# Optimization experiments

Measured on AMD Instinct MI355X. Metric: run time of the kernel, lower is better.

The kernel has to match this reference:

```python
import jax, jax.numpy as jnp
import numpy as np
from jax import lax

B, L, D_MODEL = 4, 512, 256
N_LAYERS = 6
EXPAND = 2
D_INNER = EXPAND * D_MODEL  # 512
D_STATE = 16
D_CONV = 4
DT_RANK = (D_MODEL + 15) // 16  # 16
EPS = 1e-5


def silu(x):
    return x * jax.nn.sigmoid(x)


def rmsnorm(x, w):
    var = jnp.mean(x * x, axis=-1, keepdims=True)
    return x * lax.rsqrt(var + EPS) * w


def setup_inputs() -> dict:
    key = jax.random.key(0)
    ks = jax.random.split(key, 12)
    s = lambda *sh: 0.02
    inp = {
        "x": jax.random.normal(ks[0], (B, L, D_MODEL), dtype=jnp.float32),
        "norm_w": jnp.ones((N_LAYERS, D_MODEL), jnp.float32),
        "W_in": jax.random.normal(ks[1], (N_LAYERS, 2 * D_INNER, D_MODEL), jnp.float32) * 0.02,
        "b_in": jnp.zeros((N_LAYERS, 2 * D_INNER), jnp.float32),
        "conv_w": jax.random.normal(ks[2], (N_LAYERS, D_INNER, D_CONV), jnp.float32) * 0.2,
        "W_x": jax.random.normal(ks[3], (N_LAYERS, DT_RANK + 2 * D_STATE, D_INNER), jnp.float32) * 0.02,
        "dt_w": jax.random.normal(ks[4], (N_LAYERS, D_INNER, DT_RANK), jnp.float32) * 0.1,
        "dt_b": jax.random.uniform(ks[5], (N_LAYERS, D_INNER), jnp.float32, -4.0, -2.0),
        "A_log": jnp.log(jnp.broadcast_to(jnp.arange(1, D_STATE + 1, dtype=jnp.float32), (N_LAYERS, D_INNER, D_STATE))),
        "D": jnp.ones((N_LAYERS, D_INNER), jnp.float32),
        "W_out": jax.random.normal(ks[6], (N_LAYERS, D_MODEL, D_INNER), jnp.float32) * 0.02,
        "b_out": jnp.zeros((N_LAYERS, D_MODEL), jnp.float32),
    }
    return inp


def mamba_block(x, W_in, b_in, conv_w, W_x, dt_w, dt_b, A_log, D, W_out, b_out):
    # input projection -> (B, L, 2*d_inner)
    xz = jnp.einsum("bld,ed->ble", x, W_in) + b_in
    xin, z = xz[..., :D_INNER], xz[..., D_INNER:]
    # depthwise causal conv over time (groups = d_inner, left pad d_conv-1)
    xc = lax.conv_general_dilated(
        xin.transpose(0, 2, 1),            # (B, C, L)
        conv_w[:, None, :],                # (C, 1, K)
        window_strides=(1,),
        padding=[(D_CONV - 1, 0)],
        feature_group_count=D_INNER,
        dimension_numbers=("NCH", "OIH", "NCH"),
    ).transpose(0, 2, 1)
    u = silu(xc)                           # (B, L, d_inner)
    # data-dependent dt, B, C
    xdbc = jnp.einsum("bld,rd->blr", u, W_x)
    dt = xdbc[..., :DT_RANK]
    Bm = xdbc[..., DT_RANK:DT_RANK + D_STATE]
    Cm = xdbc[..., DT_RANK + D_STATE:]
    delta = jax.nn.softplus(jnp.einsum("blr,dr->bld", dt, dt_w) + dt_b)
    A = -jnp.exp(A_log)                    # (d_inner, d_state)
    dA = jnp.exp(jnp.einsum("bld,dn->bldn", delta, A))
    dBu = jnp.einsum("bld,bln->bldn", delta * u, Bm)
    # selective scan over time
    def step(h, inp):
        dA_t, dBu_t, C_t = inp
        h = dA_t * h + dBu_t               # (B, d_inner, d_state)
        y_t = jnp.einsum("bdn,bn->bd", h, C_t)
        return h, y_t
    h0 = jnp.zeros((B, D_INNER, D_STATE), x.dtype)
    _, ys = lax.scan(step, h0, (dA.transpose(1, 0, 2, 3), dBu.transpose(1, 0, 2, 3), Cm.transpose(1, 0, 2)))
    y = ys.transpose(1, 0, 2) + u * D      # skip connection D*u
    y = y * silu(z)
    return jnp.einsum("bld,md->blm", y, W_out) + b_out


def reference(x, norm_w, W_in, b_in, conv_w, W_x, dt_w, dt_b, A_log, D, W_out, b_out):
    for i in range(N_LAYERS):
        x = x + mamba_block(rmsnorm(x, norm_w[i]), W_in[i], b_in[i], conv_w[i], W_x[i], dt_w[i], dt_b[i], A_log[i], D[i], W_out[i], b_out[i])
    return x
```

## Files before the change

### kernel.cpp

```cpp
#include <hip/hip_runtime.h>
#include <hip/hip_bf16.h>

#define B_SZ 4
#define L_SZ 512
#define D_MODEL 256
#define D_INNER 512
#define D_STATE 16
#define DT_RANK 16
#define N_LAYERS 6
#define BL (B_SZ * L_SZ)

typedef __bf16 bf16_t;
typedef __bf16 bf16x8 __attribute__((ext_vector_type(8)));
typedef __bf16 bf16x4 __attribute__((ext_vector_type(4)));
typedef float  f32x4  __attribute__((ext_vector_type(4)));

__device__ __forceinline__ float row_allreduce16(float x)
{
    int v;
    v = __builtin_amdgcn_mov_dpp(__float_as_int(x), 0x121, 0xf, 0xf, true);
    x += __int_as_float(v);
    v = __builtin_amdgcn_mov_dpp(__float_as_int(x), 0x122, 0xf, 0xf, true);
    x += __int_as_float(v);
    v = __builtin_amdgcn_mov_dpp(__float_as_int(x), 0x124, 0xf, 0xf, true);
    x += __int_as_float(v);
    v = __builtin_amdgcn_mov_dpp(__float_as_int(x), 0x128, 0xf, 0xf, true);
    x += __int_as_float(v);
    return x;
}

__global__ __launch_bounds__(256) void cast3_kernel(
    const float* __restrict__ s0, const float* __restrict__ s1,
    const float* __restrict__ s2, bf16_t* __restrict__ dst,
    int n0, int n1, int n2)
{
    int i = blockIdx.x * 256 + threadIdx.x;
    const float* s; int off;
    if (i < n0)            { s = s0; off = i; }
    else if (i < n0 + n1)  { s = s1; off = i - n0; }
    else if (i < n0+n1+n2) { s = s2; off = i - n0 - n1; }
    else return;
    const float4 v = *(const float4*)(s + (size_t)off * 4);
    bf16x4 o;
    o[0] = (bf16_t)v.x; o[1] = (bf16_t)v.y;
    o[2] = (bf16_t)v.z; o[3] = (bf16_t)v.w;
    *(bf16x4*)(dst + (size_t)i * 4) = o;
}

__global__ __launch_bounds__(256) void rmsnorm_kernel(
    const float* __restrict__ x, const float* __restrict__ w,
    bf16_t* __restrict__ o)
{
    int row  = blockIdx.x * 4 + (threadIdx.x >> 6);
    int lane = threadIdx.x & 63;
    const float4 v = *(const float4*)(x + (size_t)row * D_MODEL + lane * 4);
    float ss = v.x * v.x + v.y * v.y + v.z * v.z + v.w * v.w;
    #pragma unroll
    for (int off = 32; off; off >>= 1) ss += __shfl_xor(ss, off);
    float rs = rsqrtf(ss * (1.f / D_MODEL) + 1e-5f);
    const float4 wv = *(const float4*)(w + lane * 4);
    bf16x4 ov;
    ov[0] = (bf16_t)(v.x * rs * wv.x);
    ov[1] = (bf16_t)(v.y * rs * wv.y);
    ov[2] = (bf16_t)(v.z * rs * wv.z);
    ov[3] = (bf16_t)(v.w * rs * wv.w);
    *(bf16x4*)(o + (size_t)row * D_MODEL + lane * 4) = ov;
}

template<int WM, int WN, int TM_T, int TN_T, int HAS_BIAS, int HAS_RES, int ZSPLIT>
__global__ __launch_bounds__(64 * WM * WN) void gemm_mfma_nt(
    const bf16_t* __restrict__ A, int lda,
    const bf16_t* __restrict__ Bw, int ldb,
    const float* __restrict__ bias,
    const float* __restrict__ R, int ldr,
    float* __restrict__ C, int ldc,
    float* __restrict__ Z,
    int K)
{
    constexpr int BK = 64;
    constexpr int BM = WM * TM_T * 16;
    constexpr int BN = WN * TN_T * 16;
    constexpr int NT = 64 * WM * WN;
    constexpr int LDK = BK + 8;
    __shared__ bf16_t As[BM][LDK];
    __shared__ bf16_t Bs[BN][LDK];

    const int tid  = threadIdx.x;
    const int wave = tid >> 6, lane = tid & 63;
    const int wm = wave / WN, wn = wave % WN;
    const int lm = lane & 15, quad = lane >> 4;
    const int m0 = blockIdx.y * BM, n0 = blockIdx.x * BN;

    f32x4 acc[TM_T][TN_T] = {};

    for (int k0 = 0; k0 < K; k0 += BK) {
        #pragma unroll
        for (int i = tid; i < BM * (BK / 8); i += NT) {
            int r = i >> 3, c8 = i & 7;
            *(bf16x8*)&As[r][c8 * 8] =
                *(const bf16x8*)(A + (size_t)(m0 + r) * lda + k0 + c8 * 8);
        }
        #pragma unroll
        for (int i = tid; i < BN * (BK / 8); i += NT) {
            int r = i >> 3, c8 = i & 7;
            *(bf16x8*)&Bs[r][c8 * 8] =
                *(const bf16x8*)(Bw + (size_t)(n0 + r) * ldb + k0 + c8 * 8);
        }
        __syncthreads();
        #pragma unroll
        for (int ks = 0; ks < BK / 32; ++ks) {
            bf16x8 af[TM_T], bfr[TN_T];
            #pragma unroll
            for (int i = 0; i < TM_T; ++i)
                af[i] = *(const bf16x8*)&As[wm * TM_T * 16 + i * 16 + lm][ks * 32 + quad * 8];
            #pragma unroll
            for (int j = 0; j < TN_T; ++j)
                bfr[j] = *(const bf16x8*)&Bs[wn * TN_T * 16 + j * 16 + lm][ks * 32 + quad * 8];
            #pragma unroll
            for (int i = 0; i < TM_T; ++i)
                #pragma unroll
                for (int j = 0; j < TN_T; ++j)
                    acc[i][j] = __builtin_amdgcn_mfma_f32_16x16x32_bf16(
                        af[i], bfr[j], acc[i][j], 0, 0, 0);
        }
        __syncthreads();
    }

    if (ZSPLIT && n0 >= D_INNER) {
        #pragma unroll
        for (int i = 0; i < TM_T; ++i) {
            int rowbase = m0 + wm * TM_T * 16 + i * 16 + quad * 4;
            #pragma unroll
            for (int j = 0; j < TN_T; ++j) {
                int col = n0 + wn * TN_T * 16 + j * 16 + lm;
                float4 o;
                #pragma unroll
                for (int r = 0; r < 4; ++r) {
                    float v = acc[i][j][r];
                    if (HAS_BIAS) v += bias[col];
                    ((float*)&o)[r] = v / (1.f + __expf(-v));
                }
                *(float4*)(Z + (size_t)(col - D_INNER) * BL + rowbase) = o;
            }
        }
        return;
    }

    #pragma unroll
    for (int i = 0; i < TM_T; ++i) {
        #pragma unroll
        for (int j = 0; j < TN_T; ++j) {
            int col = n0 + wn * TN_T * 16 + j * 16 + lm;
            #pragma unroll
            for (int r = 0; r < 4; ++r) {
                int rowm = m0 + wm * TM_T * 16 + i * 16 + quad * 4 + r;
                float v = acc[i][j][r];
                if (HAS_BIAS) v += bias[col];
                if (HAS_RES)  v += R[(size_t)rowm * ldr + col];
                C[(size_t)rowm * ldc + col] = v;
            }
        }
    }
}

__global__ __launch_bounds__(256) void wx_conv_kernel(
    const float* __restrict__ xzx,
    const float* __restrict__ cw,
    const bf16_t* __restrict__ Bw,
    float* __restrict__ uT,
    float* __restrict__ xdbcT)
{
    constexpr int K = 512;
    __shared__ float  xs[19][516];
    __shared__ bf16_t us[16][520];
    __shared__ f32x4  part[4][3][64];

    const int tid  = threadIdx.x;
    const int wave = tid >> 6, lane = tid & 63;
    const int lm = lane & 15, quad = lane >> 4;
    const int m0 = blockIdx.x * 16;

    for (int q = tid; q < 19 * 128; q += 256) {
        int rx = q >> 7, c4 = (q & 127) * 4;
        int mr = m0 - 3 + rx;
        float4 v = make_float4(0.f, 0.f, 0.f, 0.f);
        if (mr >= 0) v = *(const float4*)(xzx + (size_t)mr * K + c4);
        *(float4*)&xs[rx][c4] = v;
    }
    __syncthreads();

    #pragma unroll
    for (int it = 0; it < 8; ++it) {
        int item = tid + it * 256;
        int d = item >> 2, rg = item & 3;
        const float4 wv = *(const float4*)(cw + d * 4);
        float4 o;
        #pragma unroll
        for (int e = 0; e < 4; ++e) {
            int ro = rg * 4 + e;
            int t  = (m0 + ro) & (L_SZ - 1);
            float a = wv.w * xs[ro + 3][d];
            if (t >= 1) a += wv.z * xs[ro + 2][d];
            if (t >= 2) a += wv.y * xs[ro + 1][d];
            if (t >= 3) a += wv.x * xs[ro + 0][d];
            a = a / (1.f + __expf(-a));
            ((float*)&o)[e] = a;
            us[ro][d] = (bf16_t)a;
        }
        *(float4*)(uT + (size_t)d * BL + m0 + rg * 4) = o;
    }
    __syncthreads();

    f32x4 acc[3] = {};
    const int kb = wave * 128 + quad * 8;
    #pragma unroll
    for (int ks = 0; ks < 4; ++ks) {
        int k0 = kb + ks * 32;
        bf16x8 af = *(const bf16x8*)&us[lm][k0];
        #pragma unroll
        for (int j = 0; j < 3; ++j) {
            bf16x8 bfr = *(const bf16x8*)(Bw + (size_t)(j * 16 + lm) * K + k0);
            acc[j] = __builtin_amdgcn_mfma_f32_16x16x32_bf16(af, bfr, acc[j], 0, 0, 0);
        }
    }
    #pragma unroll
    for (int j = 0; j < 3; ++j) part[wave][j][lane] = acc[j];
    __syncthreads();

    if (tid < 192) {
        int j = tid >> 6, l = tid & 63;
        f32x4 s = part[0][j][l];
        s += part[1][j][l];
        s += part[2][j][l];
        s += part[3][j][l];
        int col = j * 16 + (l & 15);
        float4 v = make_float4(s[0], s[1], s[2], s[3]);
        *(float4*)(xdbcT + (size_t)col * BL + m0 + (l >> 4) * 4) = v;
    }
}

__global__ __launch_bounds__(1024, 4) void scan_kernel(
    const float* __restrict__ xdbcT,
    const float* __restrict__ uT,
    const float* __restrict__ szT,
    const float* __restrict__ dt_w,
    const float* __restrict__ dt_b,
    const float* __restrict__ A_log,
    const float* __restrict__ Dv,
    bf16_t* __restrict__ y)
{
    constexpr int TC = 32;
    constexpr int NW = L_SZ / TC;

    int blk  = blockIdx.x;
    int b    = blk >> 7;
    int dg   = blk & 127;
    int wave = threadIdx.x >> 6;
    int lane = threadIdx.x & 63;
    int d    = dg * 4 + (lane >> 4);
    int n    = lane & 15;

    __shared__ float lds_Ap[NW][64];
    __shared__ float lds_he[NW][64];

    float Adn = -__expf(A_log[d * D_STATE + n]);
    float Dd  = Dv[d];
    int r0 = b * L_SZ + wave * TC;

    const float* Brow = xdbcT  + (size_t)(DT_RANK + n) * BL;
    const float* Crow = xdbcT  + (size_t)(DT_RANK + D_STATE + n) * BL;
    const float* urow = uT     + (size_t)d * BL;
    const float* zrow = szT    + (size_t)d * BL;

    float myd[2];
    {
        float w16[16];
        #pragma unroll
        for (int k4 = 0; k4 < 4; ++k4) {
            float4 wv = *(const float4*)(dt_w + (size_t)d * 16 + k4 * 4);
            w16[k4*4+0] = wv.x; w16[k4*4+1] = wv.y;
            w16[k4*4+2] = wv.z; w16[k4*4+3] = wv.w;
        }
        float bdt = dt_b[d];
        #pragma unroll
        for (int g = 0; g < 2; ++g) {
            int t = r0 + g * 16 + n;
            float a = bdt;
            #pragma unroll
            for (int k = 0; k < 16; ++k)
                a += xdbcT[(size_t)k * BL + t] * w16[k];
            myd[g] = (a > 20.f) ? a : __logf(1.f + __expf(a));
        }
    }
    const int sbase = lane & 48;

    float hl[TC], Pl[TC];
    float h = 0.f, P = 1.f;
    #pragma unroll
    for (int g = 0; g < 2; ++g) {
        #pragma unroll
        for (int j4 = 0; j4 < 4; ++j4) {
            int rb = r0 + g * 16 + j4 * 4;
            f32x4 Bv = *(const f32x4*)(Brow + rb);
            f32x4 uv = *(const f32x4*)(urow + rb);
            float dA[4], dBu[4];
            #pragma unroll
            for (int k = 0; k < 4; ++k) {
                float dlj = __shfl(myd[g], sbase | (j4 * 4 + k));
                dA[k]  = __expf(dlj * Adn);
                dBu[k] = dlj * uv[k] * Bv[k];
            }
            #pragma unroll
            for (int k = 0; k < 4; ++k) {
                int t = g * 16 + j4 * 4 + k;
                h = dA[k] * h + dBu[k];
                P *= dA[k];
                hl[t] = h;
                Pl[t] = P;
            }
        }
    }
    lds_Ap[wave][lane] = P;
    lds_he[wave][lane] = h;
    __syncthreads();

    float H = 0.f;
    for (int j = 0; j < wave; ++j)
        H = lds_Ap[j][lane] * H + lds_he[j][lane];

    #pragma unroll
    for (int t0 = 0; t0 < TC; t0 += 16) {
        float py[16];
        #pragma unroll
        for (int j4 = 0; j4 < 4; ++j4) {
            int rb = r0 + t0 + j4 * 4;
            f32x4 Cc = *(const f32x4*)(Crow + rb);
            #pragma unroll
            for (int k = 0; k < 4; ++k) {
                int t = t0 + j4 * 4 + k;
                py[j4*4+k] = (hl[t] + Pl[t] * H) * Cc[k];
            }
        }
        #pragma unroll
        for (int j = 0; j < 16; ++j)
            py[j] = row_allreduce16(py[j]);
        if (n == 0) {
            #pragma unroll
            for (int j4 = 0; j4 < 4; ++j4) {
                int rb = r0 + t0 + j4 * 4;
                f32x4 uv = *(const f32x4*)(urow + rb);
                f32x4 sz = *(const f32x4*)(zrow + rb);
                #pragma unroll
                for (int k = 0; k < 4; ++k) {
                    int row = rb + k;
                    y[(size_t)row * D_INNER + d] =
                        (bf16_t)((py[j4*4+k] + uv[k] * Dd) * sz[k]);
                }
            }
        }
    }
}

extern "C" void kernel_launch(void* const* d_in, const int* in_sizes, int n_in,
                              void* d_out, int out_size, void* d_ws, size_t ws_size,
                              hipStream_t stream)
{
    const float* x_in   = (const float*)d_in[0];
    const float* norm_w = (const float*)d_in[1];
    const float* W_in   = (const float*)d_in[2];
    const float* b_in   = (const float*)d_in[3];
    const float* conv_w = (const float*)d_in[4];
    const float* W_x    = (const float*)d_in[5];
    const float* dt_w   = (const float*)d_in[6];
    const float* dt_b   = (const float*)d_in[7];
    const float* A_log  = (const float*)d_in[8];
    const float* Dv     = (const float*)d_in[9];
    const float* W_out  = (const float*)d_in[10];
    const float* b_out  = (const float*)d_in[11];
    float* out = (float*)d_out;

    float* ws     = (float*)d_ws;
    float* xz     = ws;
    float* uT     = xz     + BL * D_INNER;
    float* szT    = uT     + D_INNER * BL;
    float* xdbcT  = szT    + D_INNER * BL;
    bf16_t* bws   = (bf16_t*)(xdbcT + 48 * BL);
    bf16_t* xn_bf = bws;
    bf16_t* y_bf  = xn_bf + BL * D_MODEL;
    bf16_t* Wi_bf = y_bf  + BL * D_INNER;
    bf16_t* Wx_bf = Wi_bf + N_LAYERS * 2 * D_INNER * D_MODEL;
    bf16_t* Wo_bf = Wx_bf + N_LAYERS * 48 * D_INNER;

    {
        int n0 = N_LAYERS * 2 * D_INNER * D_MODEL / 4;
        int n1 = N_LAYERS * 48 * D_INNER / 4;
        int n2 = N_LAYERS * D_MODEL * D_INNER / 4;
        cast3_kernel<<<(n0 + n1 + n2 + 255) / 256, 256, 0, stream>>>(
            W_in, W_x, W_out, Wi_bf, n0, n1, n2);
    }

    for (int i = 0; i < N_LAYERS; ++i) {
        const float* xcur = (i == 0) ? x_in : out;

        rmsnorm_kernel<<<BL / 4, 256, 0, stream>>>(xcur, norm_w + i * D_MODEL, xn_bf);

        gemm_mfma_nt<2, 2, 2, 2, 1, 0, 1><<<dim3(1024 / 64, 2048 / 64), 256, 0, stream>>>(
            xn_bf, D_MODEL, Wi_bf + (size_t)i * 2 * D_INNER * D_MODEL, D_MODEL,
            b_in + i * 2 * D_INNER, nullptr, 0, xz, D_INNER, szT, D_MODEL);

        wx_conv_kernel<<<BL / 16, 256, 0, stream>>>(
            xz, conv_w + i * D_INNER * 4,
            Wx_bf + (size_t)i * 48 * D_INNER, uT, xdbcT);

        scan_kernel<<<512, 1024, 0, stream>>>(
            xdbcT, uT, szT,
            dt_w + (size_t)i * D_INNER * DT_RANK, dt_b + i * D_INNER,
            A_log + (size_t)i * D_INNER * D_STATE, Dv + i * D_INNER, y_bf);

        gemm_mfma_nt<2, 2, 2, 2, 1, 1, 0><<<dim3(256 / 64, 2048 / 64), 256, 0, stream>>>(
            y_bf, D_INNER, Wo_bf + (size_t)i * D_MODEL * D_INNER, D_INNER,
            b_out + i * D_MODEL, xcur, D_MODEL, out, D_MODEL, nullptr, D_INNER);
    }
}
```

Baseline: 487.7 us.

## Fuse next-layer RMSNorm into W_out projection epilogue

Replaces the generic W_out GEMM with a dedicated kernel in which each block computes a full 16-row strip of all 256 output columns. With whole rows in hand, the block applies the residual and bias, then computes the next layer's RMSNorm and writes the bf16 normalized activations. This removes the separate per-layer rmsnorm launch and its extra pass over the activations. The cost is that every block reloads the entire W_out tile set, and each wave has a smaller MFMA workload.

After: 504.7 us. +3.5%, slower.

```diff
diff --git a/kernel.cpp b/kernel.cpp
--- a/kernel.cpp
+++ b/kernel.cpp
@@ -67,12 +67,11 @@
     *(bf16x4*)(o + (size_t)row * D_MODEL + lane * 4) = ov;
 }
 
-template<int WM, int WN, int TM_T, int TN_T, int HAS_BIAS, int HAS_RES, int ZSPLIT>
-__global__ __launch_bounds__(64 * WM * WN) void gemm_mfma_nt(
+template<int WM, int WN, int TM_T, int TN_T>
+__global__ __launch_bounds__(64 * WM * WN) void gemm_win(
     const bf16_t* __restrict__ A, int lda,
     const bf16_t* __restrict__ Bw, int ldb,
     const float* __restrict__ bias,
-    const float* __restrict__ R, int ldr,
     float* __restrict__ C, int ldc,
     float* __restrict__ Z,
     int K)
@@ -126,7 +125,7 @@
         __syncthreads();
     }
 
-    if (ZSPLIT && n0 >= D_INNER) {
+    if (n0 >= D_INNER) {
         #pragma unroll
         for (int i = 0; i < TM_T; ++i) {
             int rowbase = m0 + wm * TM_T * 16 + i * 16 + quad * 4;
@@ -136,8 +135,7 @@
                 float4 o;
                 #pragma unroll
                 for (int r = 0; r < 4; ++r) {
-                    float v = acc[i][j][r];
-                    if (HAS_BIAS) v += bias[col];
+                    float v = acc[i][j][r] + bias[col];
                     ((float*)&o)[r] = v / (1.f + __expf(-v));
                 }
                 *(float4*)(Z + (size_t)(col - D_INNER) * BL + rowbase) = o;
@@ -154,12 +152,92 @@
             #pragma unroll
             for (int r = 0; r < 4; ++r) {
                 int rowm = m0 + wm * TM_T * 16 + i * 16 + quad * 4 + r;
-                float v = acc[i][j][r];
-                if (HAS_BIAS) v += bias[col];
-                if (HAS_RES)  v += R[(size_t)rowm * ldr + col];
-                C[(size_t)rowm * ldc + col] = v;
-            }
-        }
+                C[(size_t)rowm * ldc + col] = acc[i][j][r] + bias[col];
+            }
+        }
+    }
+}
+
+template<int NORM>
+__global__ __launch_bounds__(256) void wout_norm_kernel(
+    const bf16_t* __restrict__ A,
+    const bf16_t* __restrict__ Bw,
+    const float* __restrict__ bias,
+    const float* __restrict__ R,
+    const float* __restrict__ nw,
+    float* __restrict__ out,
+    bf16_t* __restrict__ xn)
+{
+    constexpr int K = 512, BK = 64;
+    __shared__ bf16_t As[16][K + 8];
+    __shared__ bf16_t Bs[256][BK + 8];
+    __shared__ float  ot[16][260];
+
+    const int tid  = threadIdx.x;
+    const int wn   = tid >> 6;
+    const int lane = tid & 63;
+    const int lm = lane & 15, quad = lane >> 4;
+    const int m0 = blockIdx.x * 16;
+
+    #pragma unroll
+    for (int i = tid; i < 16 * (K / 8); i += 256) {
+        int r = i >> 6, c8 = i & 63;
+        *(bf16x8*)&As[r][c8 * 8] =
+            *(const bf16x8*)(A + (size_t)(m0 + r) * K + c8 * 8);
+    }
+
+    f32x4 acc[4] = {};
+    for (int k0 = 0; k0 < K; k0 += BK) {
+        #pragma unroll
+        for (int i = tid; i < 256 * (BK / 8); i += 256) {
+            int r = i >> 3, c8 = i & 7;
+            *(bf16x8*)&Bs[r][c8 * 8] =
+                *(const bf16x8*)(Bw + (size_t)r * K + k0 + c8 * 8);
+        }
+        __syncthreads();
+        #pragma unroll
+        for (int ks = 0; ks < 2; ++ks) {
+            bf16x8 af = *(const bf16x8*)&As[lm][k0 + ks * 32 + quad * 8];
+            #pragma unroll
+            for (int j = 0; j < 4; ++j) {
+                bf16x8 bfr = *(const bf16x8*)&Bs[wn * 64 + j * 16 + lm][ks * 32 + quad * 8];
+                acc[j] = __builtin_amdgcn_mfma_f32_16x16x32_bf16(af, bfr, acc[j], 0, 0, 0);
+            }
+        }
+        __syncthreads();
+    }
+
+    #pragma unroll
+    for (int j = 0; j < 4; ++j) {
+        int col = wn * 64 + j * 16 + lm;
+        float bv = bias[col];
+        #pragma unroll
+        for (int r = 0; r < 4; ++r) {
+            int row = quad * 4 + r;
+            float v = acc[j][r] + bv + R[(size_t)(m0 + row) * D_MODEL + col];
+            out[(size_t)(m0 + row) * D_MODEL + col] = v;
+            ot[row][col] = v;
+        }
+    }
+    if (NORM) {
+        __syncthreads();
+        int row = tid >> 4, c0 = (tid & 15) * 16;
+        float ss = 0.f;
+        #pragma unroll
+        for (int k = 0; k < 16; ++k) {
+            float v = ot[row][c0 + k];
+            ss += v * v;
+        }
+        ss = row_allreduce16(ss);
+        float rs = rsqrtf(ss * (1.f / D_MODEL) + 1e-5f);
+        bf16x8 o0, o1;
+        #pragma unroll
+        for (int k = 0; k < 8; ++k) {
+            o0[k] = (bf16_t)(ot[row][c0 + k]     * rs * nw[c0 + k]);
+            o1[k] = (bf16_t)(ot[row][c0 + 8 + k] * rs * nw[c0 + 8 + k]);
+        }
+        *(bf16x8*)(xn + (size_t)(m0 + row) * D_MODEL + c0)     = o0;
+        *(bf16x8*)(xn + (size_t)(m0 + row) * D_MODEL + c0 + 8) = o1;
     }
 }
 
@@ -399,14 +477,14 @@
             W_in, W_x, W_out, Wi_bf, n0, n1, n2);
     }
 
+    rmsnorm_kernel<<<BL / 4, 256, 0, stream>>>(x_in, norm_w, xn_bf);
+
     for (int i = 0; i < N_LAYERS; ++i) {
         const float* xcur = (i == 0) ? x_in : out;
 
-        rmsnorm_kernel<<<BL / 4, 256, 0, stream>>>(xcur, norm_w + i * D_MODEL, xn_bf);
-
-        gemm_mfma_nt<2, 2, 2, 2, 1, 0, 1><<<dim3(1024 / 64, 2048 / 64), 256, 0, stream>>>(
+        gemm_win<2, 2, 2, 2><<<dim3(1024 / 64, 2048 / 64), 256, 0, stream>>>(
             xn_bf, D_MODEL, Wi_bf + (size_t)i * 2 * D_INNER * D_MODEL, D_MODEL,
-            b_in + i * 2 * D_INNER, nullptr, 0, xz, D_INNER, szT, D_MODEL);
+            b_in + i * 2 * D_INNER, xz, D_INNER, szT, D_MODEL);
 
         wx_conv_kernel<<<BL / 16, 256, 0, stream>>>(
             xz, conv_w + i * D_INNER * 4,
@@ -417,8 +495,15 @@
             dt_w + (size_t)i * D_INNER * DT_RANK, dt_b + i * D_INNER,
             A_log + (size_t)i * D_INNER * D_STATE, Dv + i * D_INNER, y_bf);
 
-        gemm_mfma_nt<2, 2, 2, 2, 1, 1, 0><<<dim3(256 / 64, 2048 / 64), 256, 0, stream>>>(
-            y_bf, D_INNER, Wo_bf + (size_t)i * D_MODEL * D_INNER, D_INNER,
-            b_out + i * D_MODEL, xcur, D_MODEL, out, D_MODEL, nullptr, D_INNER);
-    }
-}
+        if (i < N_LAYERS - 1) {
+            wout_norm_kernel<1><<<BL / 16, 256, 0, stream>>>(
+                y_bf, Wo_bf + (size_t)i * D_MODEL * D_INNER,
+                b_out + i * D_MODEL, xcur, norm_w + (i + 1) * D_MODEL,
+                out, xn_bf);
+        } else {
+            wout_norm_kernel<0><<<BL / 16, 256, 0, stream>>>(
+                y_bf, Wo_bf + (size_t)i * D_MODEL * D_INNER,
+                b_out + i * D_MODEL, xcur, nullptr, out, nullptr);
+        }
+    }
+}
```
